# Kernel tuning notes

Measured on AMD Instinct MI355X. Metric: run time of the kernel, lower is better.

Reference implementation:

```python
import jax, jax.numpy as jnp
import numpy as np

B, T, IN, H, L, OUT = 128, 512, 1024, 1024, 2, 20


def setup_inputs() -> dict:
    key = jax.random.key(0)
    ks = jax.random.split(key, 7)
    std = 1.0 / np.sqrt(H)
    x = jax.random.normal(ks[0], (B, T, IN), dtype=jnp.float32)
    # Stacked per-layer weights (layer0 input == hidden so stacking is valid)
    Wx = jax.random.uniform(ks[1], (L, 4 * H, IN), jnp.float32, -std, std)
    bx = jax.random.uniform(ks[2], (L, 4 * H), jnp.float32, -std, std)
    Wh = jax.random.uniform(ks[3], (L, 4 * H, H), jnp.float32, -std, std)
    bh = jax.random.uniform(ks[4], (L, 4 * H), jnp.float32, -std, std)
    Wout = jax.random.uniform(ks[5], (OUT, H), jnp.float32, -std, std)
    bout = jax.random.uniform(ks[6], (OUT,), jnp.float32, -std, std)
    return {"x": x, "Wx": Wx, "bx": bx, "Wh": Wh, "bh": bh, "Wout": Wout, "bout": bout}


def reference(x, Wx, bx, Wh, bh, Wout, bout):
    L = Wx.shape[0]
    H = Wh.shape[-1]
    B = x.shape[0]

    # NOTE: faithful to the source bug — c_t is rebound to tanh(cell_gate),
    # so the previous cell state is never read: cy = tanh(g)*(sig(f)+sig(i)).
    # The (write-only) cell state is therefore dropped from the carry.
    def step(h, x_t):  # h: [L,B,H], x_t: [B,IN]
        inp = x_t
        new_h = []
        for l in range(L):  # small fixed layer loop
            gates = inp @ Wx[l].T + bx[l] + h[l] @ Wh[l].T + bh[l]  # [B,4H]
            i, f, g, o = jnp.split(gates, 4, axis=1)
            cy = jnp.tanh(g) * (jax.nn.sigmoid(f) + jax.nn.sigmoid(i))
            hy = jnp.tanh(cy) * jax.nn.sigmoid(o)
            new_h.append(hy)
            inp = hy
        return jnp.stack(new_h), inp  # carry, per-step top-layer output

    h0 = jnp.zeros((L, B, H), dtype=x.dtype)
    _, outs = jax.lax.scan(step, h0, jnp.swapaxes(x, 0, 1))  # outs: [T,B,H]
    return outs[-1] @ Wout.T + bout  # linear applied to last timestep only
```

## Files before the change

### kernel.cpp

```cpp
#include <hip/hip_runtime.h>
#include <hip/hip_fp16.h>

#define TT   512
#define BB   128
#define HH   1024
#define K4   4096
#define KK   2048
#define NWG  256
#define NSLOT (TT + 2)
#define CSTRIDE 16
#define PANEL 131072
#define NBUF 17

typedef _Float16 half8  __attribute__((ext_vector_type(8)));
typedef _Float16 half4v __attribute__((ext_vector_type(4)));
typedef float    f32x4  __attribute__((ext_vector_type(4)));

__device__ __forceinline__ float sig_f(float v) { return 1.f / (1.f + __expf(-v)); }
__device__ __forceinline__ float tanh_f(float v) {
    float e = __expf(2.f * v);
    return 1.f - 2.f / (e + 1.f);
}

__device__ __forceinline__ int vload(const int* p) { return *(const volatile int*)p; }


__global__ void cast_x_kernel(const float* __restrict__ x, _Float16* __restrict__ xc) {
    const long n4 = (long)BB * TT * 256;
    const long stride = (long)gridDim.x * blockDim.x;
    for (long i = (long)blockIdx.x * blockDim.x + threadIdx.x; i < n4; i += stride) {
        int  kq  = (int)(i & 255);
        long row = i >> 8;
        int  t   = (int)(row & 511);
        int  b   = (int)(row >> 9);
        const float4 v = ((const float4*)x)[i];
        half4v h;
        h[0] = (_Float16)v.x; h[1] = (_Float16)v.y;
        h[2] = (_Float16)v.z; h[3] = (_Float16)v.w;
        int k0  = kq * 4;
        int off = (((b >> 4) * 32 + (k0 >> 5)) << 9)
                + (((((k0 >> 3) & 3) << 4) | (b & 15)) << 3) + (k0 & 7);
        *(half4v*)(xc + (long)t * PANEL + off) = h;
    }
}

__global__ void init_ws(int* __restrict__ ctr, _Float16* __restrict__ h0b,
                        _Float16* __restrict__ h1b) {
    int i = blockIdx.x * blockDim.x + threadIdx.x;
    int stride = gridDim.x * blockDim.x;
    for (int j = i; j < NSLOT * CSTRIDE; j += stride) ctr[j] = 0;
    for (int j = i; j < PANEL; j += stride) {
        h0b[j] = (_Float16)0.f;
        h1b[j] = (_Float16)0.f;
    }
}

__global__ __launch_bounds__(512, 1) void lstm_main(
    const float* __restrict__ x, const _Float16* __restrict__ xc, int useXC,
    const float* __restrict__ Wx, const float* __restrict__ bx,
    const float* __restrict__ Wh, const float* __restrict__ bh,
    _Float16* __restrict__ h0, _Float16* __restrict__ h1,
    int* __restrict__ ctr)
{
    __shared__ _Float16 wlds[KK * 32];
    __shared__ float gates[BB][33];
    __shared__ float bias_s[32];

    const int tid   = threadIdx.x;
    const int wg    = blockIdx.x;
    const int layer = wg >> 7;
    const int idx   = wg & 127;
    const int wg8   = idx * 8;
    const int cBlk  = idx >> 2;
    const int ksub  = idx & 3;

    const float* WxL = Wx + (long)layer * K4 * HH;
    const float* WhL = Wh + (long)layer * K4 * HH;
    for (int e = tid; e < KK * 32; e += 512) {
        int c = e >> 11;
        int k = e & (KK - 1);
        int g = wg8 + (c & 7) + 1024 * (c >> 3);
        float v = (k < HH) ? WxL[(long)g * HH + k] : WhL[(long)g * HH + (k - HH)];
        int row = k >> 3;
        int cs  = (c & 24) | ((c ^ row) & 7);
        wlds[row * 256 + cs * 8 + (k & 7)] = (_Float16)v;
    }
    if (tid < 32) {
        int g = wg8 + (tid & 7) + 1024 * (tid >> 3);
        bias_s[tid] = bx[layer * K4 + g] + bh[layer * K4 + g];
    }
    __syncthreads();

    const int lane = tid & 63;
    const int wv   = tid >> 6;
    const int m    = lane & 15;
    const int q    = lane >> 4;
    const int arow = wv * 16 + m;

    f32x4 acc0 = {0.f, 0.f, 0.f, 0.f};
    f32x4 acc1 = {0.f, 0.f, 0.f, 0.f};

    auto gemm = [&](const _Float16* A, int kb0) {
        const _Float16* ap = A + (size_t)wv * 16384 + (size_t)lane * 8;
        for (int hb = 0; hb < 2; ++hb) {
            half8 abuf[16];
            #pragma unroll
            for (int i = 0; i < 16; ++i)
                abuf[i] = *(const half8*)(ap + (hb * 16 + i) * 512);
            #pragma unroll
            for (int i = 0; i < 16; ++i) {
                int rb = kb0 + (hb * 16 + i) * 4 + q;
                int base = rb * 256 + (((m & 8) | ((m ^ rb) & 7)) << 3);
                half8 b0 = *(const half8*)&wlds[base];
                half8 b1 = *(const half8*)&wlds[base + 128];
                acc0 = __builtin_amdgcn_mfma_f32_16x16x32_f16(abuf[i], b0, acc0, 0, 0, 0);
                acc1 = __builtin_amdgcn_mfma_f32_16x16x32_f16(abuf[i], b1, acc1, 0, 0, 0);
            }
        }
    };
    auto gemm_f32 = [&](const float* ap0) {
        const float* ap = ap0 + (long)arow * (TT * HH) + q * 8;
        #pragma unroll 4
        for (int kk = 0; kk < HH; kk += 32) {
            float4 f0 = *(const float4*)(ap + kk);
            float4 f1 = *(const float4*)(ap + kk + 4);
            half8 af;
            af[0] = (_Float16)f0.x; af[1] = (_Float16)f0.y;
            af[2] = (_Float16)f0.z; af[3] = (_Float16)f0.w;
            af[4] = (_Float16)f1.x; af[5] = (_Float16)f1.y;
            af[6] = (_Float16)f1.z; af[7] = (_Float16)f1.w;
            int rb = (kk >> 3) + q;
            int base = rb * 256 + (((m & 8) | ((m ^ rb) & 7)) << 3);
            half8 b0 = *(const half8*)&wlds[base];
            half8 b1 = *(const half8*)&wlds[base + 128];
            acc0 = __builtin_amdgcn_mfma_f32_16x16x32_f16(af, b0, acc0, 0, 0, 0);
            acc1 = __builtin_amdgcn_mfma_f32_16x16x32_f16(af, b1, acc1, 0, 0, 0);
        }
    };

    for (int s = 0; s < NSLOT; ++s) {
        const bool active = (layer == 0) ? (s < TT) : (s >= 2);
        const int h0w  = s % NBUF;
        const int h0r1 = (s + NBUF - 1) % NBUF;
        const int h0r2 = (s + NBUF - 2) % NBUF;
        const int h1w  = (s + NBUF - 2) % NBUF;
        const int h1r  = (s + NBUF - 3) % NBUF;

        acc0 = (f32x4){0.f, 0.f, 0.f, 0.f};
        acc1 = (f32x4){0.f, 0.f, 0.f, 0.f};
        if (active) {
            if (layer == 0) {
                if (useXC) gemm(xc + (long)s * PANEL, 0);
                else       gemm_f32(x + (long)s * HH);
            } else {
                gemm(h0 + (size_t)h0r2 * PANEL, 0);
            }
        }

        if (s) {
            if (tid == 0) {
                const int* cp = ctr + (s - 1) * CSTRIDE;
                while (vload(cp) < NWG) __builtin_amdgcn_s_sleep(1);
            }
            __atomic_signal_fence(__ATOMIC_SEQ_CST);
            __syncthreads();
            if ((s & 15) == 0)
                __builtin_amdgcn_fence(__ATOMIC_ACQUIRE, "agent");
        }

        if (active) {
            _Float16* outp;
            if (layer == 0) {
                gemm(h0 + (size_t)h0r1 * PANEL, 128);
                outp = h0 + (size_t)h0w * PANEL;
            } else {
                gemm(h1 + (size_t)h1r * PANEL, 128);
                outp = h1 + (size_t)h1w * PANEL;
            }

            #pragma unroll
            for (int r = 0; r < 4; ++r) {
                gates[wv * 16 + q * 4 + r][m]      = acc0[r];
                gates[wv * 16 + q * 4 + r][16 + m] = acc1[r];
            }
            __syncthreads();

            {
                int row = tid >> 2, jp = tid & 3;
                int j0 = jp * 2, j1 = j0 + 1;
                float gi0 = gates[row][j0]      + bias_s[j0];
                float gf0 = gates[row][8 + j0]  + bias_s[8 + j0];
                float gg0 = gates[row][16 + j0] + bias_s[16 + j0];
                float go0 = gates[row][24 + j0] + bias_s[24 + j0];
                float gi1 = gates[row][j1]      + bias_s[j1];
                float gf1 = gates[row][8 + j1]  + bias_s[8 + j1];
                float gg1 = gates[row][16 + j1] + bias_s[16 + j1];
                float go1 = gates[row][24 + j1] + bias_s[24 + j1];
                float hv0 = tanh_f(tanh_f(gg0) * (sig_f(gf0) + sig_f(gi0))) * sig_f(go0);
                float hv1 = tanh_f(tanh_f(gg1) * (sig_f(gf1) + sig_f(gi1))) * sig_f(go1);
                union { _Float16 f[2]; unsigned int u; } pk;
                pk.f[0] = (_Float16)hv0; pk.f[1] = (_Float16)hv1;
                int off = (((row >> 4) * 32 + cBlk) << 9)
                        + (((ksub << 4) | (row & 15)) << 3) + j0;
                *(volatile unsigned int*)(outp + off) = pk.u;
            }
        }

        __syncthreads();
        if (tid == 0) {
            __atomic_signal_fence(__ATOMIC_SEQ_CST);
            atomicAdd(ctr + s * CSTRIDE, 1);
        }
    }
}

__global__ void out_kernel(const _Float16* __restrict__ hlast,
                           const float* __restrict__ Wout,
                           const float* __restrict__ bout,
                           float* __restrict__ out) {
    int b = blockIdx.x, o = blockIdx.y;
    int lane = threadIdx.x;
    float sum = 0.f;
    for (int k = lane; k < HH; k += 64) {
        int off = (((b >> 4) * 32 + (k >> 5)) << 9)
                + (((((k >> 3) & 3) << 4) | (b & 15)) << 3) + (k & 7);
        sum += (float)hlast[off] * Wout[(long)o * HH + k];
    }
    #pragma unroll
    for (int offz = 32; offz; offz >>= 1) sum += __shfl_down(sum, offz, 64);
    if (lane == 0) out[b * 20 + o] = sum + bout[o];
}

extern "C" void kernel_launch(void* const* d_in, const int* in_sizes, int n_in,
                              void* d_out, int out_size, void* d_ws, size_t ws_size,
                              hipStream_t stream) {
    const float* x    = (const float*)d_in[0];
    const float* Wx   = (const float*)d_in[1];
    const float* bx   = (const float*)d_in[2];
    const float* Wh   = (const float*)d_in[3];
    const float* bh   = (const float*)d_in[4];
    const float* Wout = (const float*)d_in[5];
    const float* bout = (const float*)d_in[6];
    float* out = (float*)d_out;

    char* ws = (char*)d_ws;
    const size_t PB = (size_t)PANEL * sizeof(_Float16);
    int*      ctr = (int*)ws;
    _Float16* h0  = (_Float16*)(ws + 40960);
    _Float16* h1  = (_Float16*)(ws + 40960 + NBUF * PB);
    _Float16* xc  = (_Float16*)(ws + 40960 + 2 * NBUF * PB);
    size_t need_xc = 40960 + 2 * (size_t)NBUF * PB + (size_t)TT * PB;
    int useXC = (ws_size >= need_xc) ? 1 : 0;

    hipLaunchKernelGGL(init_ws, dim3(64), dim3(256), 0, stream,
                       ctr, h0 + (size_t)(NBUF - 1) * PANEL,
                       h1 + (size_t)(NBUF - 1) * PANEL);
    if (useXC)
        hipLaunchKernelGGL(cast_x_kernel, dim3(8192), dim3(256), 0, stream, x, xc);
    hipLaunchKernelGGL(lstm_main, dim3(NWG), dim3(512), 0, stream,
                       x, xc, useXC, Wx, bx, Wh, bh, h0, h1, ctr);
    hipLaunchKernelGGL(out_kernel, dim3(BB, 20), dim3(64), 0, stream,
                       h1 + (size_t)((TT - 1) % NBUF) * PANEL, Wout, bout, out);
}
```

Measured before the change: 7.002 ms.

## Replace global atomic step counter with per-workgroup progress flags polled by each wave

Swaps the single per-step atomic counter barrier for per-workgroup progress flags on padded cache lines, written with a plain volatile store. Every wave polls all 256 flags itself (four per lane) and leaves the wait with a wave vote, which removes the workgroup-wide barrier after the spin. Layer-0 workgroups now wait only for layer-1 progress within a 14-step slack, so the two layers are loosely coupled instead of moving in lockstep. The intent is to cut atomic contention and barrier latency on every timestep. The cost is much more polling traffic to L2, since every wave reads 256 flags, and the ordering still rests on volatile stores with only occasional acquire fences.

```diff
diff --git a/kernel.cpp b/kernel.cpp
--- a/kernel.cpp
+++ b/kernel.cpp
@@ -8,7 +8,7 @@
 #define KK   2048
 #define NWG  256
 #define NSLOT (TT + 2)
-#define CSTRIDE 16
+#define FSTRIDE 32
 #define PANEL 131072
 #define NBUF 17
 
@@ -23,6 +23,7 @@
 }
 
 __device__ __forceinline__ int vload(const int* p) { return *(const volatile int*)p; }
+__device__ __forceinline__ void vstore(int* p, int v) { *(volatile int*)p = v; }
 
 
 __global__ void cast_x_kernel(const float* __restrict__ x, _Float16* __restrict__ xc) {
@@ -44,11 +45,11 @@
     }
 }
 
-__global__ void init_ws(int* __restrict__ ctr, _Float16* __restrict__ h0b,
+__global__ void init_ws(int* __restrict__ flags, _Float16* __restrict__ h0b,
                         _Float16* __restrict__ h1b) {
     int i = blockIdx.x * blockDim.x + threadIdx.x;
     int stride = gridDim.x * blockDim.x;
-    for (int j = i; j < NSLOT * CSTRIDE; j += stride) ctr[j] = 0;
+    if (i < NWG * FSTRIDE) flags[i] = 0;
     for (int j = i; j < PANEL; j += stride) {
         h0b[j] = (_Float16)0.f;
         h1b[j] = (_Float16)0.f;
@@ -60,7 +61,7 @@
     const float* __restrict__ Wx, const float* __restrict__ bx,
     const float* __restrict__ Wh, const float* __restrict__ bh,
     _Float16* __restrict__ h0, _Float16* __restrict__ h1,
-    int* __restrict__ ctr)
+    int* __restrict__ flags)
 {
     __shared__ _Float16 wlds[KK * 32];
     __shared__ float gates[BB][33];
@@ -138,6 +139,12 @@
         }
     };
 
+    const int* fp0 = flags + lane * FSTRIDE;
+    const int* fp1 = flags + (lane + 64) * FSTRIDE;
+    const int* fp2 = flags + (lane + 128) * FSTRIDE;
+    const int* fp3 = flags + (lane + 192) * FSTRIDE;
+    int* myflag = flags + wg * FSTRIDE;
+
     for (int s = 0; s < NSLOT; ++s) {
         const bool active = (layer == 0) ? (s < TT) : (s >= 2);
         const int h0w  = s % NBUF;
@@ -158,12 +165,16 @@
         }
 
         if (s) {
-            if (tid == 0) {
-                const int* cp = ctr + (s - 1) * CSTRIDE;
-                while (vload(cp) < NWG) __builtin_amdgcn_s_sleep(1);
+            const int need0 = s;
+            const int need1 = (layer == 0) ? s - 14 : s;
+            for (;;) {
+                int a = vload(fp0), b = vload(fp1);
+                int c = vload(fp2), d = vload(fp3);
+                int ok = (a >= need0) & (b >= need0) & (c >= need1) & (d >= need1);
+                if (__all(ok)) break;
+                __builtin_amdgcn_s_sleep(1);
             }
             __atomic_signal_fence(__ATOMIC_SEQ_CST);
-            __syncthreads();
             if ((s & 15) == 0)
                 __builtin_amdgcn_fence(__ATOMIC_ACQUIRE, "agent");
         }
@@ -209,7 +220,7 @@
         __syncthreads();
         if (tid == 0) {
             __atomic_signal_fence(__ATOMIC_SEQ_CST);
-            atomicAdd(ctr + s * CSTRIDE, 1);
+            vstore(myflag, s + 1);
         }
     }
 }
@@ -245,7 +256,7 @@
 
     char* ws = (char*)d_ws;
     const size_t PB = (size_t)PANEL * sizeof(_Float16);
-    int*      ctr = (int*)ws;
+    int*      flags = (int*)ws;
     _Float16* h0  = (_Float16*)(ws + 40960);
     _Float16* h1  = (_Float16*)(ws + 40960 + NBUF * PB);
     _Float16* xc  = (_Float16*)(ws + 40960 + 2 * NBUF * PB);
@@ -253,12 +264,12 @@
     int useXC = (ws_size >= need_xc) ? 1 : 0;
 
     hipLaunchKernelGGL(init_ws, dim3(64), dim3(256), 0, stream,
-                       ctr, h0 + (size_t)(NBUF - 1) * PANEL,
+                       flags, h0 + (size_t)(NBUF - 1) * PANEL,
                        h1 + (size_t)(NBUF - 1) * PANEL);
     if (useXC)
         hipLaunchKernelGGL(cast_x_kernel, dim3(8192), dim3(256), 0, stream, x, xc);
     hipLaunchKernelGGL(lstm_main, dim3(NWG), dim3(512), 0, stream,
-                       x, xc, useXC, Wx, bx, Wh, bh, h0, h1, ctr);
+                       x, xc, useXC, Wx, bx, Wh, bh, h0, h1, flags);
     hipLaunchKernelGGL(out_kernel, dim3(BB, 20), dim3(64), 0, stream,
                        h1 + (size_t)((TT - 1) % NBUF) * PANEL, Wout, bout, out);
 }
```

Result: slower. 7.399 ms (+5.7%).
